# Kernel tuning notes

Hardware: AMD Instinct MI355X
Metric: run time of the kernel (lower is better)

Reference implementation:

```python
import jax, jax.numpy as jnp
import numpy as np

N_NODES = 100000


def graph_conv(x, src, dst, Wr, br, Wroot):
    # PyG GraphConv (aggr='add'): out_i = W_rel @ sum_{j in N(i)} x_j + b_rel + W_root @ x_i
    msgs = x[src]                                              # [E, F] gather
    agg = jax.ops.segment_sum(msgs, dst, num_segments=N_NODES)  # [N, F] scatter-add
    return agg @ Wr + br + x @ Wroot


def setup_inputs() -> dict:
    key = jax.random.key(0)
    k1, k2, k3, k4 = jax.random.split(key, 4)
    F = 128
    E = 600000
    x = jax.random.normal(k1, (N_NODES, F), dtype=jnp.float32)
    edge_index = jax.random.randint(k2, (2, E), 0, N_NODES, dtype=jnp.int64)
    scale = 1.0 / np.sqrt(F)
    W_rel = jax.random.normal(k3, (5, F, F), dtype=jnp.float32) * scale
    b_rel = jnp.zeros((5, F), dtype=jnp.float32)
    W_root = jax.random.normal(k4, (5, F, F), dtype=jnp.float32) * scale
    return {"x": x, "edge_index": edge_index, "W_rel": W_rel, "b_rel": b_rel, "W_root": W_root}


def reference(x, edge_index, W_rel, b_rel, W_root):
    src, dst = edge_index[0], edge_index[1]
    x1 = jax.nn.relu(graph_conv(x, src, dst, W_rel[0], b_rel[0], W_root[0]))
    x2 = jax.nn.relu(graph_conv(x1, src, dst, W_rel[1], b_rel[1], W_root[1])) + x1
    x3 = jax.nn.relu(graph_conv(x2, src, dst, W_rel[2], b_rel[2], W_root[2])) + x2
    x4 = jax.nn.relu(graph_conv(x3, src, dst, W_rel[3], b_rel[3], W_root[3])) + x3
    x5 = graph_conv(x4, src, dst, W_rel[4], b_rel[4], W_root[4]) + x4
    return x5
```

## Files before the change

kernel.cpp:

```cpp
#include <hip/hip_runtime.h>

#define NNODES 100000
#define FDIM 128
#define NLAYERS 5

typedef __bf16 bf16_t;
typedef bf16_t bf16x8 __attribute__((ext_vector_type(8)));
typedef float  f32x4  __attribute__((ext_vector_type(4)));

__device__ __forceinline__ bf16_t f2bf(float f){ return (bf16_t)f; }
__device__ __forceinline__ float bfbits_lo(unsigned u){
  unsigned b = u << 16; return __builtin_bit_cast(float, b);
}
__device__ __forceinline__ float bfbits_hi(unsigned u){
  unsigned b = u & 0xffff0000u; return __builtin_bit_cast(float, b);
}
__device__ __forceinline__ unsigned short bfb(float f){
  bf16_t b = (bf16_t)f; return __builtin_bit_cast(unsigned short, b);
}
__device__ __forceinline__ float us2f(unsigned short u){
  unsigned b = ((unsigned)u) << 16; return __builtin_bit_cast(float, b);
}

__global__ void deg_kernel(const int* __restrict__ dstv, int* __restrict__ deg, int E){
  int e = blockIdx.x*256 + threadIdx.x;
  if(e < E) atomicAdd(&deg[dstv[e]], 1);
}

__global__ void scan1_kernel(const int* __restrict__ deg, int* __restrict__ row_start,
                             int* __restrict__ sums, int n){
  __shared__ int sm[256];
  int t = threadIdx.x;
  int base = blockIdx.x*1024 + t*4;
  int v0=0,v1=0,v2=0,v3=0;
  if(base+3 < n){ int4 q = *(const int4*)(deg+base); v0=q.x; v1=q.y; v2=q.z; v3=q.w; }
  else {
    if(base   < n) v0 = deg[base];
    if(base+1 < n) v1 = deg[base+1];
    if(base+2 < n) v2 = deg[base+2];
    if(base+3 < n) v3 = deg[base+3];
  }
  int s = v0+v1+v2+v3;
  sm[t] = s;
  __syncthreads();
  for(int off=1; off<256; off<<=1){
    int y = (t>=off) ? sm[t-off] : 0;
    __syncthreads();
    sm[t] += y;
    __syncthreads();
  }
  int excl = sm[t] - s;
  if(base   < n) row_start[base]   = excl;
  if(base+1 < n) row_start[base+1] = excl+v0;
  if(base+2 < n) row_start[base+2] = excl+v0+v1;
  if(base+3 < n) row_start[base+3] = excl+v0+v1+v2;
  if(t == 255) sums[blockIdx.x] = sm[255];
}

__global__ void scan2_kernel(int* sums, int nc){
  __shared__ int sm[128];
  int t = threadIdx.x;
  int v = (t<nc) ? sums[t] : 0;
  sm[t] = v;
  __syncthreads();
  for(int off=1; off<128; off<<=1){
    int y = (t>=off) ? sm[t-off] : 0;
    __syncthreads();
    sm[t] += y;
    __syncthreads();
  }
  if(t<nc) sums[t] = sm[t] - v;
}

__global__ void scan3_kernel(int* row_start, const int* __restrict__ sums, int n, int E){
  int i = blockIdx.x*256 + threadIdx.x;
  if(i < n)       row_start[i] += sums[i>>10];
  else if(i == n) row_start[n]  = E;
}

__global__ void fill_kernel(const int* __restrict__ srcv, const int* __restrict__ dstv,
                            const int* __restrict__ row_start, int* __restrict__ cnt,
                            int* __restrict__ csr, int E){
  int e = blockIdx.x*256 + threadIdx.x;
  if(e < E){
    int d = dstv[e];
    int p = atomicAdd(&cnt[d], 1);
    csr[row_start[d] + p] = srcv[e];
  }
}

__global__ __launch_bounds__(256) void cvt_kernel(const float* __restrict__ x,
                                                  unsigned short* __restrict__ xb){
  long i = ((long)blockIdx.x*256 + threadIdx.x)*8;
  float4 q0 = *(const float4*)(x+i);
  float4 q1 = *(const float4*)(x+i+4);
  unsigned short o[8];
  o[0]=bfb(q0.x); o[1]=bfb(q0.y); o[2]=bfb(q0.z); o[3]=bfb(q0.w);
  o[4]=bfb(q1.x); o[5]=bfb(q1.y); o[6]=bfb(q1.z); o[7]=bfb(q1.w);
  *(ulong2*)(xb+i) = *(ulong2*)o;
}

__global__ __launch_bounds__(256) void gather_kernel(const unsigned short* __restrict__ xb,
                                                     const int* __restrict__ row_start,
                                                     const int* __restrict__ csr,
                                                     unsigned short* __restrict__ agg, int n){
  int wid  = (blockIdx.x*256 + threadIdx.x) >> 6;
  int lane = threadIdx.x & 63;
  if(wid >= n) return;
  int s0 = row_start[wid];
  int s1 = row_start[wid+1];
  float ax[8] = {}, ay[8] = {};
  int i = s0;
  for(; i+8 <= s1; i += 8){
    unsigned v[8];
    #pragma unroll
    for(int j=0;j<8;j++){
      int c = csr[i+j];
      v[j] = *(const unsigned*)(xb + (size_t)c*FDIM + lane*2);
    }
    #pragma unroll
    for(int j=0;j<8;j++){ ax[j] += bfbits_lo(v[j]); ay[j] += bfbits_hi(v[j]); }
  }
  if(i+4 <= s1){
    unsigned v[4];
    #pragma unroll
    for(int j=0;j<4;j++){
      int c = csr[i+j];
      v[j] = *(const unsigned*)(xb + (size_t)c*FDIM + lane*2);
    }
    #pragma unroll
    for(int j=0;j<4;j++){ ax[j] += bfbits_lo(v[j]); ay[j] += bfbits_hi(v[j]); }
    i += 4;
  }
  if(i+2 <= s1){
    unsigned v0 = *(const unsigned*)(xb + (size_t)csr[i]*FDIM + lane*2);
    unsigned v1 = *(const unsigned*)(xb + (size_t)csr[i+1]*FDIM + lane*2);
    ax[4] += bfbits_lo(v0); ay[4] += bfbits_hi(v0);
    ax[5] += bfbits_lo(v1); ay[5] += bfbits_hi(v1);
    i += 2;
  }
  if(i < s1){
    unsigned v0 = *(const unsigned*)(xb + (size_t)csr[i]*FDIM + lane*2);
    ax[6] += bfbits_lo(v0); ay[6] += bfbits_hi(v0);
  }
  float axs = ((ax[0]+ax[1])+(ax[2]+ax[3])) + ((ax[4]+ax[5])+(ax[6]+ax[7]));
  float ays = ((ay[0]+ay[1])+(ay[2]+ay[3])) + ((ay[4]+ay[5])+(ay[6]+ay[7]));
  unsigned o = (unsigned)bfb(axs) | ((unsigned)bfb(ays) << 16);
  *(unsigned*)(agg + (size_t)wid*FDIM + lane*2) = o;
}

__global__ void wprep_kernel(const float* __restrict__ Wrel, const float* __restrict__ Wroot,
                             bf16_t* __restrict__ Bp){
  int gid = blockIdx.x*256 + threadIdx.x;
  if(gid >= NLAYERS*64*64) return;
  int lane = gid & 63;
  int fg   = (gid>>6) & 63;
  int l    = gid >> 12;
  int kk = fg >> 3, cb = fg & 7;
  int kbase = kk*32 + (lane>>4)*8;
  int col   = cb*16 + (lane&15);
  bf16_t tmp[8];
  #pragma unroll
  for(int e=0;e<8;e++){
    int k = kbase + e;
    float v = (k < FDIM) ? Wrel [l*FDIM*FDIM + k*FDIM + col]
                         : Wroot[l*FDIM*FDIM + (k-FDIM)*FDIM + col];
    tmp[e] = f2bf(v);
  }
  bf16_t* o = Bp + (long)gid*8;
  #pragma unroll
  for(int e=0;e<8;e++) o[e] = tmp[e];
}

__global__ __launch_bounds__(256) void gemm_kernel(
    const bf16_t* __restrict__ Aagg, const bf16_t* __restrict__ Ain,
    const bf16_t* __restrict__ Bp, const float* __restrict__ bias,
    bf16_t* __restrict__ outB, float* __restrict__ outF,
    int relu, int resf, int ntiles){
  int lane = threadIdx.x & 63;
  int t    = (blockIdx.x*256 + threadIdx.x) >> 6;
  if(t >= ntiles) return;
  int r_lo = lane & 15;
  int kgrp = lane >> 4;
  long r0 = (long)t*16;

  const bf16_t* pa = Aagg + (r0 + r_lo)*FDIM + kgrp*8;
  const bf16_t* pi = Ain  + (r0 + r_lo)*FDIM + kgrp*8;

  f32x4 acc[8] = {};
  #pragma unroll
  for(int kk=0;kk<8;kk++){
    bf16x8 a = (kk<4) ? *(const bf16x8*)(pa + kk*32) : *(const bf16x8*)(pi + (kk-4)*32);
    #pragma unroll
    for(int cb=0;cb<8;cb++){
      bf16x8 wfr = *(const bf16x8*)(Bp + (((kk<<3)|cb)*64 + lane)*8);
      acc[cb] = __builtin_amdgcn_mfma_f32_16x16x32_bf16(wfr, a, acc[cb], 0, 0, 0);
    }
  }
  long nrow = r0 + r_lo;
  #pragma unroll
  for(int cb=0;cb<8;cb++){
    int col = cb*16 + kgrp*4;
    float4 bv = *(const float4*)(bias + col);
    float v0 = acc[cb][0] + bv.x;
    float v1 = acc[cb][1] + bv.y;
    float v2 = acc[cb][2] + bv.z;
    float v3 = acc[cb][3] + bv.w;
    if(relu){ v0=fmaxf(v0,0.f); v1=fmaxf(v1,0.f); v2=fmaxf(v2,0.f); v3=fmaxf(v3,0.f); }
    if(resf){
      ushort4 rv = *(const ushort4*)((const unsigned short*)Ain + nrow*FDIM + col);
      v0 += us2f(rv.x); v1 += us2f(rv.y); v2 += us2f(rv.z); v3 += us2f(rv.w);
    }
    if(outF){
      float4 o; o.x=v0; o.y=v1; o.z=v2; o.w=v3;
      *(float4*)(outF + nrow*FDIM + col) = o;
    } else {
      uint2 o;
      o.x = (unsigned)bfb(v0) | ((unsigned)bfb(v1) << 16);
      o.y = (unsigned)bfb(v2) | ((unsigned)bfb(v3) << 16);
      *(uint2*)((unsigned short*)outB + nrow*FDIM + col) = o;
    }
  }
}

extern "C" void kernel_launch(void* const* d_in, const int* in_sizes, int n_in,
                              void* d_out, int out_size, void* d_ws, size_t ws_size,
                              hipStream_t stream){
  const float* x     = (const float*)d_in[0];
  const int*   ei    = (const int*)  d_in[1];
  const float* Wrel  = (const float*)d_in[2];
  const float* brel  = (const float*)d_in[3];
  const float* Wroot = (const float*)d_in[4];
  float* out = (float*)d_out;

  const int N = NNODES;
  const int E = in_sizes[1] / 2;
  const int* srcv = ei;
  const int* dstv = ei + E;

  char* w = (char*)d_ws;
  auto alloc = [&](size_t b)->char*{ char* p = w; w += (b + 255) & ~(size_t)255; return p; };
  unsigned short* xb  = (unsigned short*)alloc((size_t)N*FDIM*2);
  unsigned short* h_a = (unsigned short*)alloc((size_t)N*FDIM*2);
  unsigned short* h_b = (unsigned short*)alloc((size_t)N*FDIM*2);
  unsigned short* agg = (unsigned short*)alloc((size_t)N*FDIM*2);
  int*    deg       = (int*)   alloc((size_t)N*4);
  int*    cnt       = (int*)   alloc((size_t)N*4);
  int*    row_start = (int*)   alloc((size_t)(N+1)*4);
  int*    csr       = (int*)   alloc((size_t)E*4);
  bf16_t* Bp        = (bf16_t*)alloc((size_t)NLAYERS*4096*8*2);
  int*    sums      = (int*)   alloc(512);

  hipMemsetAsync(deg, 0, (size_t)N*4, stream);
  hipMemsetAsync(cnt, 0, (size_t)N*4, stream);

  int eb = (E + 255) / 256;
  int nchunks = (N + 1023) / 1024;
  deg_kernel <<<eb, 256, 0, stream>>>(dstv, deg, E);
  scan1_kernel<<<nchunks, 256, 0, stream>>>(deg, row_start, sums, N);
  scan2_kernel<<<1, 128, 0, stream>>>(sums, nchunks);
  scan3_kernel<<<(N + 1 + 255)/256, 256, 0, stream>>>(row_start, sums, N, E);
  fill_kernel<<<eb, 256, 0, stream>>>(srcv, dstv, row_start, cnt, csr, E);
  wprep_kernel<<<(NLAYERS*4096 + 255)/256, 256, 0, stream>>>(Wrel, Wroot, Bp);
  cvt_kernel  <<<(N*FDIM/8 + 255)/256, 256, 0, stream>>>(x, xb);

  const int ntiles  = N / 16;
  const int gblocks = (ntiles + 3) / 4;

  typedef unsigned short us;
  struct Lay { const us* in; us* o; int relu; int res; };
  Lay L[5] = {
    { xb,  h_a, 1, 0 },
    { h_a, h_b, 1, 1 },
    { h_b, h_a, 1, 1 },
    { h_a, h_b, 1, 1 },
    { h_b, 0,   0, 1 },
  };
  for(int l=0; l<NLAYERS; l++){
    gather_kernel<<<N/4, 256, 0, stream>>>(L[l].in, row_start, csr, agg, N);
    gemm_kernel  <<<gblocks, 256, 0, stream>>>((const bf16_t*)agg, (const bf16_t*)L[l].in,
                                               Bp + (size_t)l*4096*8,
                                               brel + l*FDIM,
                                               (bf16_t*)L[l].o, (l==4)? out : nullptr,
                                               L[l].relu, L[l].res, ntiles);
  }
}
```

Baseline: 429.5 us.

## Fuse neighbor gather into GEMM kernel via swizzled shared-memory tile

```diff
diff --git a/kernel.cpp b/kernel.cpp
--- a/kernel.cpp
+++ b/kernel.cpp
@@ -100,55 +100,6 @@
   *(ulong2*)(xb+i) = *(ulong2*)o;
 }
 
-__global__ __launch_bounds__(256) void gather_kernel(const unsigned short* __restrict__ xb,
-                                                     const int* __restrict__ row_start,
-                                                     const int* __restrict__ csr,
-                                                     unsigned short* __restrict__ agg, int n){
-  int wid  = (blockIdx.x*256 + threadIdx.x) >> 6;
-  int lane = threadIdx.x & 63;
-  if(wid >= n) return;
-  int s0 = row_start[wid];
-  int s1 = row_start[wid+1];
-  float ax[8] = {}, ay[8] = {};
-  int i = s0;
-  for(; i+8 <= s1; i += 8){
-    unsigned v[8];
-    #pragma unroll
-    for(int j=0;j<8;j++){
-      int c = csr[i+j];
-      v[j] = *(const unsigned*)(xb + (size_t)c*FDIM + lane*2);
-    }
-    #pragma unroll
-    for(int j=0;j<8;j++){ ax[j] += bfbits_lo(v[j]); ay[j] += bfbits_hi(v[j]); }
-  }
-  if(i+4 <= s1){
-    unsigned v[4];
-    #pragma unroll
-    for(int j=0;j<4;j++){
-      int c = csr[i+j];
-      v[j] = *(const unsigned*)(xb + (size_t)c*FDIM + lane*2);
-    }
-    #pragma unroll
-    for(int j=0;j<4;j++){ ax[j] += bfbits_lo(v[j]); ay[j] += bfbits_hi(v[j]); }
-    i += 4;
-  }
-  if(i+2 <= s1){
-    unsigned v0 = *(const unsigned*)(xb + (size_t)csr[i]*FDIM + lane*2);
-    unsigned v1 = *(const unsigned*)(xb + (size_t)csr[i+1]*FDIM + lane*2);
-    ax[4] += bfbits_lo(v0); ay[4] += bfbits_hi(v0);
-    ax[5] += bfbits_lo(v1); ay[5] += bfbits_hi(v1);
-    i += 2;
-  }
-  if(i < s1){
-    unsigned v0 = *(const unsigned*)(xb + (size_t)csr[i]*FDIM + lane*2);
-    ax[6] += bfbits_lo(v0); ay[6] += bfbits_hi(v0);
-  }
-  float axs = ((ax[0]+ax[1])+(ax[2]+ax[3])) + ((ax[4]+ax[5])+(ax[6]+ax[7]));
-  float ays = ((ay[0]+ay[1])+(ay[2]+ay[3])) + ((ay[4]+ay[5])+(ay[6]+ay[7]));
-  unsigned o = (unsigned)bfb(axs) | ((unsigned)bfb(ays) << 16);
-  *(unsigned*)(agg + (size_t)wid*FDIM + lane*2) = o;
-}
-
 __global__ void wprep_kernel(const float* __restrict__ Wrel, const float* __restrict__ Wroot,
                              bf16_t* __restrict__ Bp){
   int gid = blockIdx.x*256 + threadIdx.x;
@@ -172,25 +123,73 @@
   for(int e=0;e<8;e++) o[e] = tmp[e];
 }
 
-__global__ __launch_bounds__(256) void gemm_kernel(
-    const bf16_t* __restrict__ Aagg, const bf16_t* __restrict__ Ain,
+__global__ __launch_bounds__(256) void fused_kernel(
+    const unsigned short* __restrict__ xb_in,
+    const int* __restrict__ row_start, const int* __restrict__ csr,
     const bf16_t* __restrict__ Bp, const float* __restrict__ bias,
     bf16_t* __restrict__ outB, float* __restrict__ outF,
     int relu, int resf, int ntiles){
-  int lane = threadIdx.x & 63;
-  int t    = (blockIdx.x*256 + threadIdx.x) >> 6;
+  __shared__ char As[4*4096];
+  int tid  = threadIdx.x;
+  int lane = tid & 63;
+  int t    = (blockIdx.x*256 + tid) >> 6;
   if(t >= ntiles) return;
+  char* wls = As + (tid>>6)*4096;
+  long r0 = (long)t*16;
+
+  #pragma unroll 1
+  for(int g=0; g<4; g++){
+    int rbase = (int)r0 + g*4;
+    int st0 = row_start[rbase+0], st1 = row_start[rbase+1];
+    int st2 = row_start[rbase+2], st3 = row_start[rbase+3];
+    int st4 = row_start[rbase+4];
+    int n0 = st1-st0, n1 = st2-st1, n2 = st3-st2, n3 = st4-st3;
+    float ax0=0,ay0=0,ax1=0,ay1=0,ax2=0,ay2=0,ax3=0,ay3=0;
+    int nmax = max(max(n0,n1),max(n2,n3));
+    #pragma unroll 1
+    for(int j=0;j<nmax;j++){
+      if(j<n0){ unsigned v=*(const unsigned*)(xb_in+(size_t)csr[st0+j]*FDIM+lane*2);
+                ax0+=bfbits_lo(v); ay0+=bfbits_hi(v); }
+      if(j<n1){ unsigned v=*(const unsigned*)(xb_in+(size_t)csr[st1+j]*FDIM+lane*2);
+                ax1+=bfbits_lo(v); ay1+=bfbits_hi(v); }
+      if(j<n2){ unsigned v=*(const unsigned*)(xb_in+(size_t)csr[st2+j]*FDIM+lane*2);
+                ax2+=bfbits_lo(v); ay2+=bfbits_hi(v); }
+      if(j<n3){ unsigned v=*(const unsigned*)(xb_in+(size_t)csr[st3+j]*FDIM+lane*2);
+                ax3+=bfbits_lo(v); ay3+=bfbits_hi(v); }
+    }
+    int cb4 = lane*4;
+    {
+      int rr = g*4+0; unsigned o = (unsigned)bfb(ax0) | ((unsigned)bfb(ay0)<<16);
+      *(unsigned*)(wls + rr*256 + (cb4 ^ ((rr&7)<<4))) = o;
+    }
+    {
+      int rr = g*4+1; unsigned o = (unsigned)bfb(ax1) | ((unsigned)bfb(ay1)<<16);
+      *(unsigned*)(wls + rr*256 + (cb4 ^ ((rr&7)<<4))) = o;
+    }
+    {
+      int rr = g*4+2; unsigned o = (unsigned)bfb(ax2) | ((unsigned)bfb(ay2)<<16);
+      *(unsigned*)(wls + rr*256 + (cb4 ^ ((rr&7)<<4))) = o;
+    }
+    {
+      int rr = g*4+3; unsigned o = (unsigned)bfb(ax3) | ((unsigned)bfb(ay3)<<16);
+      *(unsigned*)(wls + rr*256 + (cb4 ^ ((rr&7)<<4))) = o;
+    }
+  }
+
   int r_lo = lane & 15;
   int kgrp = lane >> 4;
-  long r0 = (long)t*16;
-
-  const bf16_t* pa = Aagg + (r0 + r_lo)*FDIM + kgrp*8;
-  const bf16_t* pi = Ain  + (r0 + r_lo)*FDIM + kgrp*8;
+  bf16x8 afr[4];
+  #pragma unroll
+  for(int kk=0;kk<4;kk++){
+    int X = kk*64 + kgrp*16;
+    afr[kk] = *(const bf16x8*)(wls + r_lo*256 + (X ^ ((r_lo&7)<<4)));
+  }
+  const bf16_t* pi = (const bf16_t*)xb_in + (r0 + r_lo)*FDIM + kgrp*8;
 
   f32x4 acc[8] = {};
   #pragma unroll
   for(int kk=0;kk<8;kk++){
-    bf16x8 a = (kk<4) ? *(const bf16x8*)(pa + kk*32) : *(const bf16x8*)(pi + (kk-4)*32);
+    bf16x8 a = (kk<4) ? afr[kk] : *(const bf16x8*)(pi + (kk-4)*32);
     #pragma unroll
     for(int cb=0;cb<8;cb++){
       bf16x8 wfr = *(const bf16x8*)(Bp + (((kk<<3)|cb)*64 + lane)*8);
@@ -208,7 +207,7 @@
     float v3 = acc[cb][3] + bv.w;
     if(relu){ v0=fmaxf(v0,0.f); v1=fmaxf(v1,0.f); v2=fmaxf(v2,0.f); v3=fmaxf(v3,0.f); }
     if(resf){
-      ushort4 rv = *(const ushort4*)((const unsigned short*)Ain + nrow*FDIM + col);
+      ushort4 rv = *(const ushort4*)(xb_in + nrow*FDIM + col);
       v0 += us2f(rv.x); v1 += us2f(rv.y); v2 += us2f(rv.z); v3 += us2f(rv.w);
     }
     if(outF){
@@ -243,7 +242,6 @@
   unsigned short* xb  = (unsigned short*)alloc((size_t)N*FDIM*2);
   unsigned short* h_a = (unsigned short*)alloc((size_t)N*FDIM*2);
   unsigned short* h_b = (unsigned short*)alloc((size_t)N*FDIM*2);
-  unsigned short* agg = (unsigned short*)alloc((size_t)N*FDIM*2);
   int*    deg       = (int*)   alloc((size_t)N*4);
   int*    cnt       = (int*)   alloc((size_t)N*4);
   int*    row_start = (int*)   alloc((size_t)(N+1)*4);
@@ -277,11 +275,10 @@
     { h_b, 0,   0, 1 },
   };
   for(int l=0; l<NLAYERS; l++){
-    gather_kernel<<<N/4, 256, 0, stream>>>(L[l].in, row_start, csr, agg, N);
-    gemm_kernel  <<<gblocks, 256, 0, stream>>>((const bf16_t*)agg, (const bf16_t*)L[l].in,
-                                               Bp + (size_t)l*4096*8,
-                                               brel + l*FDIM,
-                                               (bf16_t*)L[l].o, (l==4)? out : nullptr,
-                                               L[l].relu, L[l].res, ntiles);
-  }
-}
+    fused_kernel<<<gblocks, 256, 0, stream>>>(L[l].in, row_start, csr,
+                                              Bp + (size_t)l*4096*8,
+                                              brel + l*FDIM,
+                                              (bf16_t*)L[l].o, (l==4)? out : nullptr,
+                                              L[l].relu, L[l].res, ntiles);
+  }
+}
```

Result: slower. 792.0 us (+84.4%).

## Stage GEMM row tiles in swizzled LDS and split columns across waves

Applied to the files above, without the earlier changes.

```diff
diff --git a/kernel.cpp b/kernel.cpp
--- a/kernel.cpp
+++ b/kernel.cpp
@@ -176,39 +176,53 @@
     const bf16_t* __restrict__ Aagg, const bf16_t* __restrict__ Ain,
     const bf16_t* __restrict__ Bp, const float* __restrict__ bias,
     bf16_t* __restrict__ outB, float* __restrict__ outF,
-    int relu, int resf, int ntiles){
-  int lane = threadIdx.x & 63;
-  int t    = (blockIdx.x*256 + threadIdx.x) >> 6;
-  if(t >= ntiles) return;
+    int relu, int resf){
+  __shared__ char As[8192];
+  int tid  = threadIdx.x;
+  int lane = tid & 63;
+  int wv   = tid >> 6;
+  long tile0 = (long)blockIdx.x*16;
+
+  {
+    int row = tid >> 4, c16 = tid & 15;
+    int so  = c16*16;
+    int sw  = so ^ ((row & 7) << 4);
+    ulong2 va = *(const ulong2*)((const char*)Aagg + (tile0+row)*256 + so);
+    ulong2 vi = *(const ulong2*)((const char*)Ain  + (tile0+row)*256 + so);
+    *(ulong2*)(As + row*256 + sw)        = va;
+    *(ulong2*)(As + 4096 + row*256 + sw) = vi;
+  }
+  __syncthreads();
+
   int r_lo = lane & 15;
   int kgrp = lane >> 4;
-  long r0 = (long)t*16;
-
-  const bf16_t* pa = Aagg + (r0 + r_lo)*FDIM + kgrp*8;
-  const bf16_t* pi = Ain  + (r0 + r_lo)*FDIM + kgrp*8;
-
-  f32x4 acc[8] = {};
+  int cb0 = wv*2, cb1 = wv*2+1;
+  f32x4 acc0 = {}, acc1 = {};
   #pragma unroll
   for(int kk=0;kk<8;kk++){
-    bf16x8 a = (kk<4) ? *(const bf16x8*)(pa + kk*32) : *(const bf16x8*)(pi + (kk-4)*32);
-    #pragma unroll
-    for(int cb=0;cb<8;cb++){
-      bf16x8 wfr = *(const bf16x8*)(Bp + (((kk<<3)|cb)*64 + lane)*8);
-      acc[cb] = __builtin_amdgcn_mfma_f32_16x16x32_bf16(wfr, a, acc[cb], 0, 0, 0);
-    }
-  }
-  long nrow = r0 + r_lo;
-  #pragma unroll
-  for(int cb=0;cb<8;cb++){
+    const char* base = (kk<4) ? As : (As + 4096);
+    int X = (kk&3)*64 + kgrp*16;
+    bf16x8 a = *(const bf16x8*)(base + r_lo*256 + (X ^ ((r_lo&7)<<4)));
+    bf16x8 w0 = *(const bf16x8*)(Bp + (((kk<<3)|cb0)*64 + lane)*8);
+    bf16x8 w1 = *(const bf16x8*)(Bp + (((kk<<3)|cb1)*64 + lane)*8);
+    acc0 = __builtin_amdgcn_mfma_f32_16x16x32_bf16(w0, a, acc0, 0, 0, 0);
+    acc1 = __builtin_amdgcn_mfma_f32_16x16x32_bf16(w1, a, acc1, 0, 0, 0);
+  }
+
+  long nrow = tile0 + r_lo;
+  #pragma unroll
+  for(int h=0; h<2; h++){
+    int cb = h ? cb1 : cb0;
+    f32x4 acc = h ? acc1 : acc0;
     int col = cb*16 + kgrp*4;
     float4 bv = *(const float4*)(bias + col);
-    float v0 = acc[cb][0] + bv.x;
-    float v1 = acc[cb][1] + bv.y;
-    float v2 = acc[cb][2] + bv.z;
-    float v3 = acc[cb][3] + bv.w;
+    float v0 = acc[0] + bv.x;
+    float v1 = acc[1] + bv.y;
+    float v2 = acc[2] + bv.z;
+    float v3 = acc[3] + bv.w;
     if(relu){ v0=fmaxf(v0,0.f); v1=fmaxf(v1,0.f); v2=fmaxf(v2,0.f); v3=fmaxf(v3,0.f); }
     if(resf){
-      ushort4 rv = *(const ushort4*)((const unsigned short*)Ain + nrow*FDIM + col);
+      ushort4 rv = *(const ushort4*)(As + 4096 + r_lo*256 + ((col*2) ^ ((r_lo&7)<<4)));
       v0 += us2f(rv.x); v1 += us2f(rv.y); v2 += us2f(rv.z); v3 += us2f(rv.w);
     }
     if(outF){
@@ -251,8 +265,7 @@
   bf16_t* Bp        = (bf16_t*)alloc((size_t)NLAYERS*4096*8*2);
   int*    sums      = (int*)   alloc(512);
 
-  hipMemsetAsync(deg, 0, (size_t)N*4, stream);
-  hipMemsetAsync(cnt, 0, (size_t)N*4, stream);
+  hipMemsetAsync(deg, 0, (size_t)((char*)cnt - (char*)deg) + (size_t)N*4, stream);
 
   int eb = (E + 255) / 256;
   int nchunks = (N + 1023) / 1024;
@@ -264,8 +277,7 @@
   wprep_kernel<<<(NLAYERS*4096 + 255)/256, 256, 0, stream>>>(Wrel, Wroot, Bp);
   cvt_kernel  <<<(N*FDIM/8 + 255)/256, 256, 0, stream>>>(x, xb);
 
-  const int ntiles  = N / 16;
-  const int gblocks = (ntiles + 3) / 4;
+  const int gtiles = N / 16;
 
   typedef unsigned short us;
   struct Lay { const us* in; us* o; int relu; int res; };
@@ -278,10 +290,10 @@
   };
   for(int l=0; l<NLAYERS; l++){
     gather_kernel<<<N/4, 256, 0, stream>>>(L[l].in, row_start, csr, agg, N);
-    gemm_kernel  <<<gblocks, 256, 0, stream>>>((const bf16_t*)agg, (const bf16_t*)L[l].in,
-                                               Bp + (size_t)l*4096*8,
-                                               brel + l*FDIM,
-                                               (bf16_t*)L[l].o, (l==4)? out : nullptr,
-                                               L[l].relu, L[l].res, ntiles);
-  }
-}
+    gemm_kernel  <<<gtiles, 256, 0, stream>>>((const bf16_t*)agg, (const bf16_t*)L[l].in,
+                                              Bp + (size_t)l*4096*8,
+                                              brel + l*FDIM,
+                                              (bf16_t*)L[l].o, (l==4)? out : nullptr,
+                                              L[l].relu, L[l].res);
+  }
+}
```

New measurement: 393.0 us. 1.09x faster.
